# Performance work log

Measured on AMD Instinct MI355X. Metric: run time of the kernel, lower is better.

The kernel has to match this reference:

```python
import math
import jax, jax.numpy as jnp
import numpy as np

HIDDEN = 1024   # config.hidden_size
INTER = 4096    # config.intermediate_size
EXPERTS = 8     # config.moe_experts == config.global_experts
B, T = 4, 2048
EPS = 1e-12     # config.epsilon
CAP_FACTOR = 1.0
MIN_CAP = 4


def layer_norm(x, g, b, eps=EPS):
    m = jnp.mean(x, axis=-1, keepdims=True)
    v = jnp.var(x, axis=-1, keepdims=True)
    return (x - m) * jax.lax.rsqrt(v + eps) * g + b


def top1_gate(x, wg, capacity):
    # DeepSpeed top1gating: softmax gate, argmax expert, capacity-based token drop.
    logits = x @ wg                                    # [S, E]
    gates = jax.nn.softmax(logits, axis=-1)
    E = wg.shape[-1]
    idx = jnp.argmax(gates, axis=-1)                   # [S]
    mask1 = jax.nn.one_hot(idx, E, dtype=gates.dtype)  # [S, E]
    locations = jnp.cumsum(mask1, axis=0) - mask1      # exclusive cumsum = slot within expert
    mask1 = mask1 * (locations < capacity).astype(gates.dtype)  # drop overflow tokens
    gates1_s = jnp.sum(gates * mask1, axis=-1)         # [S] prob of chosen expert
    loc_s = jnp.sum(locations * mask1, axis=-1).astype(jnp.int32)
    loc_oh = jax.nn.one_hot(loc_s, capacity, dtype=gates.dtype)          # [S, C]
    combine = gates1_s[:, None, None] * mask1[:, :, None] * loc_oh[:, None, :]  # [S, E, C]
    dispatch = jax.lax.stop_gradient((combine > 0).astype(x.dtype))      # bool mask in torch
    return combine, dispatch


def setup_inputs() -> dict:
    key = jax.random.key(0)
    ks = jax.random.split(key, 8)
    s = 0.02
    return {
        "x": jax.random.normal(ks[0], (B, T, HIDDEN), jnp.float32),
        "attn_nw": jnp.ones((HIDDEN,), jnp.float32),
        "attn_nb": jnp.zeros((HIDDEN,), jnp.float32),
        "wg": jax.random.normal(ks[1], (HIDDEN, EXPERTS), jnp.float32) * s,
        "inter_w": jax.random.normal(ks[2], (EXPERTS, HIDDEN, INTER), jnp.float32) * s,
        "inter_b": jnp.zeros((EXPERTS, INTER), jnp.float32),
        "output_w": jax.random.normal(ks[3], (EXPERTS, INTER, HIDDEN), jnp.float32) * s,
        "output_b": jnp.zeros((EXPERTS, HIDDEN), jnp.float32),
        "res_inter_w": jax.random.normal(ks[4], (HIDDEN, INTER), jnp.float32) * s,
        "res_inter_b": jnp.zeros((INTER,), jnp.float32),
        "res_output_w": jax.random.normal(ks[5], (INTER, HIDDEN), jnp.float32) * s,
        "res_output_b": jnp.zeros((HIDDEN,), jnp.float32),
        "res_coef": jax.random.normal(ks[6], (HIDDEN, 2), jnp.float32) * s,
    }


def reference(x, attn_nw, attn_nb, wg, inter_w, inter_b, output_w, output_b,
              res_inter_w, res_inter_b, res_output_w, res_output_b, res_coef):
    Bx, Tx, M = x.shape
    S = Bx * Tx
    E = wg.shape[-1]
    capacity = max(MIN_CAP, math.ceil(S / E * CAP_FACTOR))  # static

    residual = x.reshape(S, M)                  # attention output + bias (attention = identity here)
    attn_out = layer_norm(residual, attn_nw, attn_nb)  # ds_layernorm

    # gate + dispatch: einsum_sec_sm_ecm
    combine, dispatch = top1_gate(attn_out, wg, capacity)
    dispatched = jnp.einsum('sec,sm->ecm', dispatch, attn_out)  # [E, C, M]

    # expert MLPs: fused gemm-gelu then output projection + bias
    h = jax.nn.gelu(jnp.einsum('ecm,emi->eci', dispatched, inter_w) + inter_b[:, None, :], approximate=True)
    expert_out = jnp.einsum('eci,eim->ecm', h, output_w) + output_b[:, None, :]

    # gated combine: matmul(combine.reshape(S, E*C), expert_out.reshape(E*C, M))
    moe_out = jnp.einsum('sec,ecm->sm', combine, expert_out)

    # residual-MLP branch (mlp_type == 'residual')
    rh = jax.nn.gelu(attn_out @ res_inter_w + res_inter_b, approximate=True)
    res_mlp_out = rh @ res_output_w + res_output_b
    coef = jax.nn.softmax(attn_out @ res_coef, axis=-1)          # [S, 2]
    out = res_mlp_out * coef[:, :1] + moe_out * coef[:, 1:]      # moe_res_matmul

    out = out + residual                                         # bias_residual
    return out.reshape(Bx, Tx, M)
```

## Files before the change

kernel.cpp:

```cpp
#include <hip/hip_runtime.h>
#include <hip/hip_bf16.h>
#include <type_traits>

#define S_TOK 8192
#define HID 1024
#define INTERX 4096
#define NEXP 8
#define CAPX 1024
#define MTOT 16384

using f32x4 = __attribute__((ext_vector_type(4))) float;
using bf16x8 = __attribute__((ext_vector_type(8))) short;

__device__ __forceinline__ short f2bf(float f) {
    union { float f; unsigned u; } v; v.f = f;
    unsigned r = (v.u + 0x7FFFu + ((v.u >> 16) & 1u)) >> 16;
    return (short)r;
}
__device__ __forceinline__ float bflo(int p) {
    union { unsigned u; float f; } v; v.u = (unsigned)p << 16; return v.f;
}
__device__ __forceinline__ float bfhi(int p) {
    union { unsigned u; float f; } v; v.u = (unsigned)p & 0xffff0000u; return v.f;
}

__device__ __forceinline__ float gelu_f(float x) {
    float x2 = x * x;
    float t = __expf(x * fmaf(x2, -0.07135677f, -1.5957691f));
    return x * __builtin_amdgcn_rcpf(1.0f + t);
}

__device__ __forceinline__ void gl_lds16(const short* g, short* l) {
    __builtin_amdgcn_global_load_lds(
        (const __attribute__((address_space(1))) void*)g,
        (__attribute__((address_space(3))) void*)l, 16, 0, 0);
}

template<int PERM>
__device__ __forceinline__ void convtrans_body(
    short (*tile)[72],
    const float* __restrict__ src_e, const float* __restrict__ src_r,
    short* __restrict__ dst, int K, int N, long sSrc, long sDst,
    int bxi, int byi, long z)
{
    const float* s = (z < 8) ? (src_e + z * sSrc) : src_r;
    short* d = dst + z * sDst;
    int n0 = bxi * 64, k0 = byi * 64;
    int t = threadIdx.x;
    int br = t >> 4, bc = t & 15;
    const float* sp = s + (long)(k0 + br * 4) * N + n0 + bc * 4;
    float4 r0 = *(const float4*)(sp);
    float4 r1 = *(const float4*)(sp + N);
    float4 r2 = *(const float4*)(sp + 2 * (long)N);
    float4 r3 = *(const float4*)(sp + 3 * (long)N);
    if (PERM) {
        float rr[4][4] = { {r0.x,r0.y,r0.z,r0.w}, {r1.x,r1.y,r1.z,r1.w},
                           {r2.x,r2.y,r2.z,r2.w}, {r3.x,r3.y,r3.z,r3.w} };
#pragma unroll
        for (int j = 0; j < 4; j++) {
            int kl = br * 4 + j;
            int kp = (kl & 15) * 4 + (kl >> 4);
#pragma unroll
            for (int q = 0; q < 4; q++)
                tile[bc * 4 + q][kp] = f2bf(rr[j][q]);
        }
    } else {
        short4 c0 = { f2bf(r0.x), f2bf(r1.x), f2bf(r2.x), f2bf(r3.x) };
        short4 c1 = { f2bf(r0.y), f2bf(r1.y), f2bf(r2.y), f2bf(r3.y) };
        short4 c2 = { f2bf(r0.z), f2bf(r1.z), f2bf(r2.z), f2bf(r3.z) };
        short4 c3 = { f2bf(r0.w), f2bf(r1.w), f2bf(r2.w), f2bf(r3.w) };
        *(short4*)&tile[bc * 4 + 0][br * 4] = c0;
        *(short4*)&tile[bc * 4 + 1][br * 4] = c1;
        *(short4*)&tile[bc * 4 + 2][br * 4] = c2;
        *(short4*)&tile[bc * 4 + 3][br * 4] = c3;
    }
    __syncthreads();
    int n = t >> 2, kc = (t & 3) * 16;
    int4 o0 = *(const int4*)&tile[n][kc];
    int4 o1 = *(const int4*)&tile[n][kc + 8];
    short* dp = d + (long)(n0 + n) * K + k0 + kc;
    *(int4*)(dp) = o0;
    *(int4*)(dp + 8) = o1;
}

template<int PERM>
__global__ __launch_bounds__(256) void convtrans_kernel(
    const float* __restrict__ src_e, const float* __restrict__ src_r,
    short* __restrict__ dst, int K, int N, long sSrc, long sDst)
{
    __shared__ __align__(16) short tile[64][72];
    convtrans_body<PERM>(tile, src_e, src_r, dst, K, N, sSrc, sDst,
                         blockIdx.x, blockIdx.y, (long)blockIdx.z);
}

__global__ __launch_bounds__(256) void fused_pre_kernel(
    const float* __restrict__ src_e, const float* __restrict__ src_r,
    short* __restrict__ w1t,
    const float* __restrict__ x, const float* __restrict__ nw, const float* __restrict__ nb,
    const float* __restrict__ wg, const float* __restrict__ rcf,
    short* __restrict__ attn_bf, int* __restrict__ eidx, float* __restrict__ gate,
    float* __restrict__ coef0, float* __restrict__ coef1,
    int* __restrict__ map2, int* __restrict__ zbufi)
{
    __shared__ __align__(16) short tile[64][72];
    int z = blockIdx.z;
    if (z < 9) {
        convtrans_body<0>(tile, src_e, src_r, w1t, HID, INTERX,
                          (long)HID * INTERX, (long)HID * INTERX,
                          blockIdx.x, blockIdx.y, (long)z);
        return;
    }
    int s = (z - 9) * 1024 + blockIdx.y * 64 + blockIdx.x;
    int tid = threadIdx.x;
    int lane = tid & 63, wave = tid >> 6;
    double (*gred)[10] = (double(*)[10])(&tile[0][0]);
    float  (*wred)[2]  = (float(*)[2])(&tile[32][0]);

    if (tid == 0) {
        map2[s] = -1;
        map2[NEXP * CAPX + s] = s;
    }
    if (s == 0) ((int2*)zbufi)[tid] = int2{0, 0};

    float4 xv = *(const float4*)(x + (size_t)s * HID + tid * 4);
    float sum = xv.x + xv.y + xv.z + xv.w;
    float sq  = xv.x*xv.x + xv.y*xv.y + xv.z*xv.z + xv.w*xv.w;
#pragma unroll
    for (int o = 32; o > 0; o >>= 1) {
        sum += __shfl_down(sum, o, 64);
        sq  += __shfl_down(sq, o, 64);
    }
    if (lane == 0) { wred[wave][0] = sum; wred[wave][1] = sq; }
    __syncthreads();
    float ts = wred[0][0] + wred[1][0] + wred[2][0] + wred[3][0];
    float tq = wred[0][1] + wred[1][1] + wred[2][1] + wred[3][1];
    float m  = ts * (1.0f / HID);
    float var = tq * (1.0f / HID) - m * m;
    float rs = rsqrtf(var + 1e-12f);

    float4 g4 = *(const float4*)(nw + tid * 4);
    float4 b4 = *(const float4*)(nb + tid * 4);
    float y[4];
    y[0] = (xv.x - m) * rs * g4.x + b4.x;
    y[1] = (xv.y - m) * rs * g4.y + b4.y;
    y[2] = (xv.z - m) * rs * g4.z + b4.z;
    y[3] = (xv.w - m) * rs * g4.w + b4.w;

    short4 yb = { f2bf(y[0]), f2bf(y[1]), f2bf(y[2]), f2bf(y[3]) };
    *(short4*)(attn_bf + (size_t)s * HID + tid * 4) = yb;

    double a[10];
#pragma unroll
    for (int q = 0; q < 10; q++) a[q] = 0.0;
#pragma unroll
    for (int j = 0; j < 4; j++) {
        int k = tid * 4 + j;
        float4 w0 = *(const float4*)(wg + k * 8);
        float4 w1 = *(const float4*)(wg + k * 8 + 4);
        double yj = (double)y[j];
        a[0] += yj * w0.x; a[1] += yj * w0.y; a[2] += yj * w0.z; a[3] += yj * w0.w;
        a[4] += yj * w1.x; a[5] += yj * w1.y; a[6] += yj * w1.z; a[7] += yj * w1.w;
        float2 rc = *(const float2*)(rcf + k * 2);
        a[8] += yj * rc.x; a[9] += yj * rc.y;
    }
#pragma unroll
    for (int o = 32; o > 0; o >>= 1)
#pragma unroll
        for (int q = 0; q < 10; q++) a[q] += __shfl_down(a[q], o, 64);
    if (lane == 0)
#pragma unroll
        for (int q = 0; q < 10; q++) gred[wave][q] = a[q];
    __syncthreads();
    if (tid == 0) {
        float l[8];
#pragma unroll
        for (int e = 0; e < 8; e++)
            l[e] = (float)(gred[0][e] + gred[1][e] + gred[2][e] + gred[3][e]);
        int bi = 0; float bv = l[0];
#pragma unroll
        for (int e = 1; e < 8; e++) if (l[e] > bv) { bv = l[e]; bi = e; }
        float den = 0.0f;
#pragma unroll
        for (int e = 0; e < 8; e++) den += expf(l[e] - bv);
        gate[s] = 1.0f / den;
        eidx[s] = bi;
        float r0 = (float)(gred[0][8] + gred[1][8] + gred[2][8] + gred[3][8]);
        float r1 = (float)(gred[0][9] + gred[1][9] + gred[2][9] + gred[3][9]);
        float mx = fmaxf(r0, r1);
        float e0 = expf(r0 - mx), e1 = expf(r1 - mx);
        float inv = 1.0f / (e0 + e1);
        coef0[s] = e0 * inv; coef1[s] = e1 * inv;
    }
}

__global__ __launch_bounds__(256) void assign_kernel(
    const int* __restrict__ eidx, int* __restrict__ slot, int* __restrict__ map2)
{
    int tid = threadIdx.x;
    __shared__ int se[S_TOK];
    __shared__ int cnt[2][256][NEXP];
#pragma unroll
    for (int i = 0; i < S_TOK / 4 / 256; i++)
        ((int4*)se)[tid + i * 256] = ((const int4*)eidx)[tid + i * 256];
    __syncthreads();

    int c[NEXP];
#pragma unroll
    for (int e = 0; e < NEXP; e++) c[e] = 0;
    int base = tid * 32;
#pragma unroll
    for (int q = 0; q < 8; q++) {
        int4 v = ((const int4*)se)[tid * 8 + q];
        c[v.x]++; c[v.y]++; c[v.z]++; c[v.w]++;
    }
#pragma unroll
    for (int e = 0; e < NEXP; e++) cnt[0][tid][e] = c[e];
    __syncthreads();

    int src = 0;
    for (int step = 1; step < 256; step <<= 1) {
        int dst = src ^ 1;
#pragma unroll
        for (int e = 0; e < NEXP; e++) {
            int v = cnt[src][tid][e];
            if (tid >= step) v += cnt[src][tid - step][e];
            cnt[dst][tid][e] = v;
        }
        __syncthreads();
        src = dst;
    }
    int off[NEXP];
#pragma unroll
    for (int e = 0; e < NEXP; e++) off[e] = (tid > 0) ? cnt[src][tid - 1][e] : 0;
    for (int t = 0; t < 32; t++) {
        int s = base + t;
        int e = se[s];
        int loc = off[e]++;
        if (loc < CAPX) { slot[s] = loc; map2[e * CAPX + loc] = s; }
        else            { slot[s] = -1; }
    }
}

template<int EPI, int GATHER>
__global__ __launch_bounds__(256, 2) void gemm_kernel(
    const short* __restrict__ A, const short* __restrict__ W,
    const float* __restrict__ bias_e, const float* __restrict__ bias_r,
    short* __restrict__ out, const int* __restrict__ map2,
    const short* __restrict__ zbuf, int N, int K, long sW, long sB,
    const float* __restrict__ cw_e, const float* __restrict__ cw_r,
    short* __restrict__ cdst, int nGemm)
{
    __shared__ __align__(16) short a_lds[128 * 64];
    __shared__ __align__(16) short b_lds[256 * 64];

    int bid = blockIdx.x + gridDim.x * blockIdx.y;
    if (bid >= nGemm) {
        int cid = bid - nGemm;
        convtrans_body<1>((short(*)[72])a_lds, cw_e, cw_r, cdst,
                          INTERX, HID, (long)INTERX * HID, (long)INTERX * HID,
                          cid & 15, (cid >> 4) & 63, (long)(cid >> 10));
        return;
    }

    int L = bid;
    int by = (L & 7) * 16 + ((L >> 3) & 15);
    int bx = L >> 7;

    long e = by >> 3; if (e > 8) e = 8;
    const short* Wb = W + e * sW;
    const float* biasb = (by < 64) ? (bias_e + e * sB) : bias_r;

    int tid = threadIdx.x;
    int lane = tid & 63, wave = tid >> 6;
    int wm = wave & 1, wn = wave >> 1;
    int lm = lane & 15, lq = lane >> 4;
    int lr = lane >> 3, ch = lane & 7;
    int chs = (ch ^ lr) * 8;

    const short* pA[4];
    const short* pB[8];
#pragma unroll
    for (int it = 0; it < 4; it++) {
        int row = (wave * 4 + it) * 8 + lr;
        if (GATHER) {
            int s = map2[by * 128 + row];
            pA[it] = (s >= 0) ? (A + (long)s * K) : zbuf;
        } else {
            pA[it] = A + ((long)by * 128 + row) * K;
        }
    }
#pragma unroll
    for (int it = 0; it < 8; it++) {
        int row = (wave * 8 + it) * 8 + lr;
        pB[it] = Wb + ((long)bx * 256 + row) * K;
    }

    f32x4 acc[4][8];
#pragma unroll
    for (int i = 0; i < 4; i++)
#pragma unroll
        for (int j = 0; j < 8; j++) acc[i][j] = { 0.f, 0.f, 0.f, 0.f };

    for (int kb = 0; kb < K; kb += 64) {
#pragma unroll
        for (int it = 0; it < 4; it++)
            gl_lds16(pA[it] + kb + chs, a_lds + (wave * 4 + it) * 512);
#pragma unroll
        for (int it = 0; it < 8; it++)
            gl_lds16(pB[it] + kb + chs, b_lds + (wave * 8 + it) * 512);
        __syncthreads();
#pragma unroll
        for (int ks = 0; ks < 64; ks += 32) {
            int po = ((lq ^ (lm & 7)) * 8) ^ ks;
            bf16x8 af[4], bfr[8];
#pragma unroll
            for (int i = 0; i < 4; i++)
                af[i] = *(const bf16x8*)(a_lds + (wm * 64 + i * 16 + lm) * 64 + po);
#pragma unroll
            for (int j = 0; j < 8; j++)
                bfr[j] = *(const bf16x8*)(b_lds + (wn * 128 + j * 16 + lm) * 64 + po);
#pragma unroll
            for (int i = 0; i < 4; i++)
#pragma unroll
                for (int j = 0; j < 8; j++)
                    acc[i][j] = __builtin_amdgcn_mfma_f32_16x16x32_bf16(af[i], bfr[j], acc[i][j], 0, 0, 0);
        }
        __syncthreads();
    }

    float bb[8];
#pragma unroll
    for (int j = 0; j < 8; j++)
        bb[j] = biasb[bx * 256 + wn * 128 + j * 16 + lm];

#pragma unroll
    for (int i = 0; i < 4; i++) {
#pragma unroll
        for (int r = 0; r < 4; r++) {
            long row = (long)by * 128 + wm * 64 + i * 16 + lq * 4 + r;
            if (EPI == 1) {
                short* rp = out + row * N + bx * 256 + wn * 128;
#pragma unroll
                for (int h = 0; h < 2; h++) {
                    int b0 = f2bf(gelu_f(acc[i][h*4+0][r] + bb[h*4+0]));
                    int b1 = f2bf(gelu_f(acc[i][h*4+1][r] + bb[h*4+1]));
                    int b2 = f2bf(gelu_f(acc[i][h*4+2][r] + bb[h*4+2]));
                    int b3 = f2bf(gelu_f(acc[i][h*4+3][r] + bb[h*4+3]));
                    int2 pk;
                    pk.x = (b0 & 0xFFFF) | (b1 << 16);
                    pk.y = (b2 & 0xFFFF) | (b3 << 16);
                    *(int2*)(rp + h * 64 + lm * 4) = pk;
                }
            } else {
#pragma unroll
                for (int j = 0; j < 8; j++) {
                    int col = bx * 256 + wn * 128 + j * 16 + lm;
                    out[row * N + col] = f2bf(acc[i][j][r] + bb[j]);
                }
            }
        }
    }
}

__global__ __launch_bounds__(256) void final_kernel(
    const float* __restrict__ x, const short* __restrict__ eout2,
    const int* __restrict__ eidx, const int* __restrict__ slot,
    const float* __restrict__ gate, const float* __restrict__ coef0,
    const float* __restrict__ coef1, float* __restrict__ out)
{
    int s = blockIdx.x, tid = threadIdx.x;
    float c0 = coef0[s], g = gate[s] * coef1[s];
    int sl = slot[s], e = eidx[s];
    float4 xv = *(const float4*)(x + (size_t)s * HID + tid * 4);
    int2 rm = *(const int2*)(eout2 + ((size_t)(NEXP * CAPX + s)) * HID + tid * 4);
    int2 mo = { 0, 0 };
    if (sl >= 0) mo = *(const int2*)(eout2 + ((size_t)(e * CAPX + sl)) * HID + tid * 4);
    float4 o;
    o.x = bflo(rm.x) * c0 + g * bflo(mo.x) + xv.x;
    o.y = bfhi(rm.x) * c0 + g * bfhi(mo.x) + xv.y;
    o.z = bflo(rm.y) * c0 + g * bflo(mo.y) + xv.z;
    o.w = bfhi(rm.y) * c0 + g * bfhi(mo.y) + xv.w;
    *(float4*)(out + (size_t)s * HID + tid * 4) = o;
}

extern "C" void kernel_launch(void* const* d_in, const int* in_sizes, int n_in,
                              void* d_out, int out_size, void* d_ws, size_t ws_size,
                              hipStream_t stream) {
    const float* x           = (const float*)d_in[0];
    const float* attn_nw     = (const float*)d_in[1];
    const float* attn_nb     = (const float*)d_in[2];
    const float* wg          = (const float*)d_in[3];
    const float* inter_w     = (const float*)d_in[4];
    const float* inter_b     = (const float*)d_in[5];
    const float* output_w    = (const float*)d_in[6];
    const float* output_b    = (const float*)d_in[7];
    const float* res_inter_w = (const float*)d_in[8];
    const float* res_inter_b = (const float*)d_in[9];
    const float* res_output_w= (const float*)d_in[10];
    const float* res_output_b= (const float*)d_in[11];
    const float* res_coef    = (const float*)d_in[12];
    float* out = (float*)d_out;

    char* ws = (char*)d_ws;
    size_t off = 0;
    auto alloc = [&](size_t bytes) { void* p = ws + off; off += (bytes + 255) & ~(size_t)255; return p; };
    char* region1 = (char*)alloc((size_t)MTOT * HID * 2);
    short* wreg   = (short*)alloc((size_t)9 * HID * INTERX * 2);
    short* hbuf2  = (short*)alloc((size_t)MTOT * INTERX * 2);
    int*   eidx   = (int*)alloc(S_TOK * 4);
    int*   slot   = (int*)alloc(S_TOK * 4);
    float* gate   = (float*)alloc(S_TOK * 4);
    float* c0     = (float*)alloc(S_TOK * 4);
    float* c1     = (float*)alloc(S_TOK * 4);
    int*   map2   = (int*)alloc(MTOT * 4);
    short* zbuf   = (short*)alloc(1024 * 2);

    size_t off_base = off;
    short* w2t_sep = (short*)alloc((size_t)9 * HID * INTERX * 2);
    bool sep = (off <= ws_size);
    short* w2t = sep ? w2t_sep : wreg;
    if (!sep) off = off_base;

    short* attn_bf = (short*)region1;
    short* eout2   = (short*)region1;
    short* w1t = wreg;

    fused_pre_kernel<<<dim3(64, 16, 17), 256, 0, stream>>>(
        inter_w, res_inter_w, w1t,
        x, attn_nw, attn_nb, wg, res_coef,
        attn_bf, eidx, gate, c0, c1, map2, (int*)zbuf);

    assign_kernel<<<1, 256, 0, stream>>>(eidx, slot, map2);

    const int NG1 = (MTOT / 128) * (INTERX / 256);

    if (sep) {
        gemm_kernel<1, 1><<<dim3(NG1 + 9216), 256, 0, stream>>>(
            attn_bf, w1t, inter_b, res_inter_b, hbuf2, map2, zbuf,
            INTERX, HID, (long)HID*INTERX, INTERX,
            output_w, res_output_w, w2t, NG1);
    } else {
        gemm_kernel<1, 1><<<dim3(NG1), 256, 0, stream>>>(
            attn_bf, w1t, inter_b, res_inter_b, hbuf2, map2, zbuf,
            INTERX, HID, (long)HID*INTERX, INTERX,
            nullptr, nullptr, nullptr, NG1);
        convtrans_kernel<1><<<dim3(HID/64, INTERX/64, 9), 256, 0, stream>>>(
            output_w, res_output_w, w2t, INTERX, HID,
            (long)INTERX*HID, (long)INTERX*HID);
    }

    const int NG2 = (MTOT / 128) * (HID / 256);
    gemm_kernel<0, 0><<<dim3(NG2), 256, 0, stream>>>(
        hbuf2, w2t, output_b, res_output_b, eout2, nullptr, zbuf,
        HID, INTERX, (long)INTERX*HID, HID,
        nullptr, nullptr, nullptr, NG2);

    final_kernel<<<S_TOK, 256, 0, stream>>>(x, eout2, eidx, slot, gate, c0, c1, out);

    (void)in_sizes; (void)n_in; (void)out_size;
}
```

Measured before the change: 714.4 us.

## Add 256x256 8-wave GEMM for output projection and interleave convtrans blocks

Replaces the second GEMM (output projection, K=4096) with a new 512-thread kernel that uses 256x256 tiles, 128KB of LDS double-buffered in quarter stages, and a priority/barrier schedule that overlaps MFMA with global-to-LDS loads. It also interleaves the weight-transpose blocks with the first GEMM's tiles (8 GEMM blocks per 36 convert blocks) instead of appending them at the end of the grid. The larger tile is meant to raise arithmetic intensity and reduce redundant loads. The interleaving is meant to balance memory-bound and compute-bound work across the GPU. The cost is higher register and LDS pressure and only 256 blocks for the second GEMM, which may under-fill the device.

```diff
diff --git a/kernel.cpp b/kernel.cpp
--- a/kernel.cpp
+++ b/kernel.cpp
@@ -241,25 +241,32 @@
     }
 }
 
-template<int EPI, int GATHER>
+template<int EPI, int GATHER, int ILV>
 __global__ __launch_bounds__(256, 2) void gemm_kernel(
     const short* __restrict__ A, const short* __restrict__ W,
     const float* __restrict__ bias_e, const float* __restrict__ bias_r,
     short* __restrict__ out, const int* __restrict__ map2,
     const short* __restrict__ zbuf, int N, int K, long sW, long sB,
     const float* __restrict__ cw_e, const float* __restrict__ cw_r,
-    short* __restrict__ cdst, int nGemm)
+    short* __restrict__ cdst)
 {
     __shared__ __align__(16) short a_lds[128 * 64];
     __shared__ __align__(16) short b_lds[256 * 64];
 
-    int bid = blockIdx.x + gridDim.x * blockIdx.y;
-    if (bid >= nGemm) {
-        int cid = bid - nGemm;
-        convtrans_body<1>((short(*)[72])a_lds, cw_e, cw_r, cdst,
-                          INTERX, HID, (long)INTERX * HID, (long)INTERX * HID,
-                          cid & 15, (cid >> 4) & 63, (long)(cid >> 10));
-        return;
+    int bid;
+    if (ILV) {
+        int raw = blockIdx.x;
+        int chunk = raw / 44, pos = raw - chunk * 44;
+        if (pos >= 8) {
+            int cid = chunk * 36 + (pos - 8);
+            convtrans_body<1>((short(*)[72])a_lds, cw_e, cw_r, cdst,
+                              INTERX, HID, (long)INTERX * HID, (long)INTERX * HID,
+                              cid & 15, (cid >> 4) & 63, (long)(cid >> 10));
+            return;
+        }
+        bid = chunk * 8 + pos;
+    } else {
+        bid = blockIdx.x + gridDim.x * blockIdx.y;
     }
 
     int L = bid;
@@ -355,6 +362,173 @@
 #pragma unroll
                 for (int j = 0; j < 8; j++) {
                     int col = bx * 256 + wn * 128 + j * 16 + lm;
+                    out[row * N + col] = f2bf(acc[i][j][r] + bb[j]);
+                }
+            }
+        }
+    }
+}
+
+template<int EPI, int GATHER>
+__global__ __launch_bounds__(512, 2) void gemm8_kernel(
+    const short* __restrict__ A, const short* __restrict__ W,
+    const float* __restrict__ bias_e, const float* __restrict__ bias_r,
+    short* __restrict__ out, const int* __restrict__ map2,
+    const short* __restrict__ zbuf, int N, int K, long sW, long sB)
+{
+    __shared__ __align__(16) short lds[65536];
+
+    int L = blockIdx.x;
+    int by = (L & 7) * 8 + ((L >> 3) & 7);
+    int bx = L >> 6;
+
+    long e = by >> 2; if (e > 8) e = 8;
+    const short* Wb = W + e * sW;
+    const float* biasb = (by < 32) ? (bias_e + e * sB) : bias_r;
+
+    int tid = threadIdx.x;
+    int lane = tid & 63, wave = tid >> 6;
+    int wm = wave & 1, wn = wave >> 1;
+    int lm = lane & 15, lq = lane >> 4;
+    int lr = lane >> 3, ch = lane & 7;
+    int chs = (ch ^ lr) * 8;
+
+    const short* pA[4];
+    const short* pAb = nullptr;
+    if (GATHER) {
+#pragma unroll
+        for (int h = 0; h < 2; h++)
+#pragma unroll
+            for (int it = 0; it < 2; it++) {
+                int rt = h * 128 + (wave * 2 + it) * 8 + lr;
+                int s = map2[by * 256 + rt];
+                pA[h * 2 + it] = ((s >= 0) ? (A + (long)s * K) : zbuf) + chs;
+            }
+    } else {
+        pAb = A + ((long)by * 256 + wave * 16 + lr) * K + chs;
+    }
+    const short* pBb = Wb + ((long)bx * 256 + wave * 16 + lr) * K + chs;
+
+#define A_SRC(h,it,t) (GATHER ? (pA[(h)*2+(it)] + (t)*64) \
+                              : (pAb + ((h)*128 + (it)*8)*(long)K + (t)*64))
+#define B_SRC(h,it,t) (pBb + ((h)*128 + (it)*8)*(long)K + (t)*64)
+#define STAGE_A(b,h,t) do { \
+    gl_lds16(A_SRC(h,0,t), lds + (b)*32768 + (h)*8192 + wave*1024); \
+    gl_lds16(A_SRC(h,1,t), lds + (b)*32768 + (h)*8192 + wave*1024 + 512); } while (0)
+#define STAGE_B(b,h,t) do { \
+    gl_lds16(B_SRC(h,0,t), lds + (b)*32768 + 16384 + (h)*8192 + wave*1024); \
+    gl_lds16(B_SRC(h,1,t), lds + (b)*32768 + 16384 + (h)*8192 + wave*1024 + 512); } while (0)
+#define LOAD_A(QM) do { _Pragma("unroll") \
+    for (int i2 = 0; i2 < 4; i2++) { \
+        const short* ap = base + (QM)*8192 + wm*4096 + i2*1024 + lm*64; \
+        af[i2][0] = *(const bf16x8*)(ap + po0); \
+        af[i2][1] = *(const bf16x8*)(ap + po1); } } while (0)
+#define LOAD_B(QN,DST) do { _Pragma("unroll") \
+    for (int j2 = 0; j2 < 2; j2++) { \
+        const short* bp = base + 16384 + (QN)*8192 + wn*2048 + j2*1024 + lm*64; \
+        DST[j2][0] = *(const bf16x8*)(bp + po0); \
+        DST[j2][1] = *(const bf16x8*)(bp + po1); } } while (0)
+#define MFMA_Q(QM,QN,BSRC) do { _Pragma("unroll") \
+    for (int i2 = 0; i2 < 4; i2++) { _Pragma("unroll") \
+    for (int j2 = 0; j2 < 2; j2++) { \
+        f32x4 t0 = acc[(QM)*4+i2][(QN)*2+j2]; \
+        t0 = __builtin_amdgcn_mfma_f32_16x16x32_bf16(af[i2][0], BSRC[j2][0], t0, 0, 0, 0); \
+        t0 = __builtin_amdgcn_mfma_f32_16x16x32_bf16(af[i2][1], BSRC[j2][1], t0, 0, 0, 0); \
+        acc[(QM)*4+i2][(QN)*2+j2] = t0; } } } while (0)
+#define SYNC_IN do { \
+    __builtin_amdgcn_sched_barrier(0); \
+    __builtin_amdgcn_s_barrier(); \
+    asm volatile("s_waitcnt lgkmcnt(0)" ::: "memory"); \
+    __builtin_amdgcn_sched_barrier(0); \
+    __builtin_amdgcn_s_setprio(1); } while (0)
+#define SYNC_OUT do { \
+    __builtin_amdgcn_s_setprio(0); \
+    __builtin_amdgcn_sched_barrier(0); \
+    __builtin_amdgcn_s_barrier(); \
+    __builtin_amdgcn_sched_barrier(0); } while (0)
+
+    int po0 = (lq ^ (lm & 7)) * 8;
+    int po1 = po0 ^ 32;
+
+    f32x4 acc[8][4];
+#pragma unroll
+    for (int i = 0; i < 8; i++)
+#pragma unroll
+        for (int j = 0; j < 4; j++) acc[i][j] = { 0.f, 0.f, 0.f, 0.f };
+
+    const int NT = K >> 6;
+
+    STAGE_A(0, 0, 0); STAGE_B(0, 0, 0);
+    STAGE_A(0, 1, 0); STAGE_B(0, 1, 0);
+    STAGE_A(1, 0, 1); STAGE_B(1, 0, 1);
+    __builtin_amdgcn_sched_barrier(0);
+    asm volatile("s_waitcnt vmcnt(4)" ::: "memory");
+    __builtin_amdgcn_s_barrier();
+    __builtin_amdgcn_sched_barrier(0);
+
+    bf16x8 af[4][2], b0v[2][2], b1v[2][2];
+
+    for (int tt = 0; tt < NT; ++tt) {
+        const int cur = tt & 1, nxt = cur ^ 1;
+        const bool s1 = (tt + 1 < NT), s2 = (tt + 2 < NT);
+        const short* base = lds + cur * 32768;
+
+        LOAD_A(0); LOAD_B(0, b0v);
+        if (s1) STAGE_A(nxt, 1, tt + 1);
+        SYNC_IN;  MFMA_Q(0, 0, b0v);  SYNC_OUT;
+
+        LOAD_B(1, b1v);
+        if (s1) STAGE_B(nxt, 1, tt + 1);
+        SYNC_IN;  MFMA_Q(0, 1, b1v);  SYNC_OUT;
+
+        LOAD_A(1);
+        if (s2) STAGE_A(cur, 0, tt + 2);
+        SYNC_IN;  MFMA_Q(1, 0, b0v);  SYNC_OUT;
+
+        if (s2) STAGE_B(cur, 0, tt + 2);
+        SYNC_IN;  MFMA_Q(1, 1, b1v);
+        __builtin_amdgcn_s_setprio(0);
+        __builtin_amdgcn_sched_barrier(0);
+        if (s2)      { asm volatile("s_waitcnt vmcnt(4)" ::: "memory"); }
+        else if (s1) { asm volatile("s_waitcnt vmcnt(0)" ::: "memory"); }
+        __builtin_amdgcn_s_barrier();
+        __builtin_amdgcn_sched_barrier(0);
+    }
+
+#undef A_SRC
+#undef B_SRC
+#undef STAGE_A
+#undef STAGE_B
+#undef LOAD_A
+#undef LOAD_B
+#undef MFMA_Q
+#undef SYNC_IN
+#undef SYNC_OUT
+
+    float bb[4];
+#pragma unroll
+    for (int j = 0; j < 4; j++)
+        bb[j] = biasb[bx * 256 + (j >> 1) * 128 + wn * 32 + (j & 1) * 16 + lm];
+
+#pragma unroll
+    for (int i = 0; i < 8; i++) {
+        long rowb = (long)by * 256 + (i >> 2) * 128 + wm * 64 + (i & 3) * 16 + lq * 4;
+#pragma unroll
+        for (int r = 0; r < 4; r++) {
+            long row = rowb + r;
+            if (EPI == 1) {
+                short* rp = out + row * N + bx * 256;
+#pragma unroll
+                for (int jj = 0; jj < 2; jj++) {
+                    int b0 = f2bf(gelu_f(acc[i][jj * 2 + 0][r] + bb[jj * 2 + 0]));
+                    int b1 = f2bf(gelu_f(acc[i][jj * 2 + 1][r] + bb[jj * 2 + 1]));
+                    int pk = (b0 & 0xFFFF) | (b1 << 16);
+                    *(int*)(rp + (jj * 2 + (wn >> 1)) * 64 + lm * 4 + (wn & 1) * 2) = pk;
+                }
+            } else {
+#pragma unroll
+                for (int j = 0; j < 4; j++) {
+                    int col = bx * 256 + (j >> 1) * 128 + wn * 32 + (j & 1) * 16 + lm;
                     out[row * N + col] = f2bf(acc[i][j][r] + bb[j]);
                 }
             }
@@ -435,25 +609,23 @@
     const int NG1 = (MTOT / 128) * (INTERX / 256);
 
     if (sep) {
-        gemm_kernel<1, 1><<<dim3(NG1 + 9216), 256, 0, stream>>>(
+        gemm_kernel<1, 1, 1><<<dim3(NG1 + 9216), 256, 0, stream>>>(
             attn_bf, w1t, inter_b, res_inter_b, hbuf2, map2, zbuf,
             INTERX, HID, (long)HID*INTERX, INTERX,
-            output_w, res_output_w, w2t, NG1);
+            output_w, res_output_w, w2t);
     } else {
-        gemm_kernel<1, 1><<<dim3(NG1), 256, 0, stream>>>(
+        gemm_kernel<1, 1, 0><<<dim3(NG1), 256, 0, stream>>>(
             attn_bf, w1t, inter_b, res_inter_b, hbuf2, map2, zbuf,
             INTERX, HID, (long)HID*INTERX, INTERX,
-            nullptr, nullptr, nullptr, NG1);
+            nullptr, nullptr, nullptr);
         convtrans_kernel<1><<<dim3(HID/64, INTERX/64, 9), 256, 0, stream>>>(
             output_w, res_output_w, w2t, INTERX, HID,
             (long)INTERX*HID, (long)INTERX*HID);
     }
 
-    const int NG2 = (MTOT / 128) * (HID / 256);
-    gemm_kernel<0, 0><<<dim3(NG2), 256, 0, stream>>>(
+    gemm8_kernel<0, 0><<<dim3((MTOT/256) * (HID/256)), 512, 0, stream>>>(
         hbuf2, w2t, output_b, res_output_b, eout2, nullptr, zbuf,
-        HID, INTERX, (long)INTERX*HID, HID,
-        nullptr, nullptr, nullptr, NG2);
+        HID, INTERX, (long)INTERX*HID, HID);
 
     final_kernel<<<S_TOK, 256, 0, stream>>>(x, eout2, eidx, slot, gate, c0, c1, out);
 
```

After: 707.1 us. About the same (-1.0%).
